# Kernel tuning notes

Measured on AMD Instinct MI355X. Metric: run time of the kernel, lower is better.

The kernel has to match this reference:

```python
import jax, jax.numpy as jnp
import numpy as np

B, D, H = 65536, 3, 256  # collocation batch, coord dim, hidden width


def setup_inputs() -> dict:
    key = jax.random.key(0)
    ks = jax.random.split(key, 8)

    def init(k, shape, fan_in):
        return jax.random.normal(k, shape, dtype=jnp.float32) * np.float32(1.0 / np.sqrt(fan_in))

    return {
        "x": jax.random.uniform(ks[0], (B, D), dtype=jnp.float32, minval=0.1, maxval=1.0),
        "W0": init(ks[1], (D, H), D), "b0": jnp.zeros((H,), jnp.float32),
        "W1": init(ks[2], (H, H), H), "b1": jnp.zeros((H,), jnp.float32),
        "W2": init(ks[3], (H, H), H), "b2": jnp.zeros((H,), jnp.float32),
        "W3": init(ks[4], (H, H), H), "b3": jnp.zeros((H,), jnp.float32),
        "Wout": init(ks[5], (H, 1), H), "bout": jnp.zeros((1,), jnp.float32),
    }


def reference(x, W0, b0, W1, b1, W2, b2, W3, b3, Wout, bout):
    # Scalar PINN network u(xi), xi: [D]
    def u_fn(xi):
        h = jnp.tanh(xi @ W0 + b0)
        h = jnp.tanh(h @ W1 + b1)
        h = jnp.tanh(h @ W2 + b2)
        h = jnp.tanh(h @ W3 + b3)
        return (h @ Wout + bout)[0]

    u = jax.vmap(u_fn)(x)                               # [B]
    # batch_gradient: du/dx_i for every coordinate axis (Cartesian: no adjustment)
    grads = jax.vmap(jax.grad(u_fn))(x)                 # [B, D]
    # batch_hessian diagonal: d^2u/dx_i^2 via forward-over-reverse
    hess_fn = jax.jacfwd(jax.grad(u_fn))                # [D, D] per sample
    hess_diag = jax.vmap(lambda xi: jnp.diagonal(hess_fn(xi)))(x)  # [B, D]
    # pack (u, grad, hessian-diagonal) as the PDE-residual ingredients
    return jnp.concatenate([u[:, None], grads, hess_diag], axis=1)  # [B, 1+D+D]
```

## Files before the change

kernel.cpp:

```cpp
#include <hip/hip_runtime.h>
#include <hip/hip_fp16.h>

#define HDIM 256
#define MS 16
#define LDAK 264
#define CSTRIDE (MS * LDAK * 2)

typedef _Float16 half8 __attribute__((ext_vector_type(8)));
typedef _Float16 half4 __attribute__((ext_vector_type(4)));
typedef _Float16 half2v __attribute__((ext_vector_type(2)));
typedef float f32x4 __attribute__((ext_vector_type(4)));

__device__ __forceinline__ float fast_tanh(float x) {
    float e = __expf(2.0f * x);
    return 1.0f - 2.0f * __builtin_amdgcn_rcpf(e + 1.0f);
}

__device__ __forceinline__ half4 cvt4(float a, float b, float c, float d) {
    half2v lo = __builtin_bit_cast(half2v, __builtin_amdgcn_cvt_pkrtz(a, b));
    half2v hi = __builtin_bit_cast(half2v, __builtin_amdgcn_cvt_pkrtz(c, d));
    half4 r; r[0] = lo[0]; r[1] = lo[1]; r[2] = hi[0]; r[3] = hi[1];
    return r;
}

__device__ __forceinline__ void barrier_lds() {
    asm volatile("s_waitcnt lgkmcnt(0)\n\ts_barrier" ::: "memory");
}

__global__ __launch_bounds__(256) void pack_weights(const float* __restrict__ W1,
                                                    const float* __restrict__ W2,
                                                    const float* __restrict__ W3,
                                                    _Float16* __restrict__ out) {
    int tid = blockIdx.x * 256 + threadIdx.x;
    int l = tid >> 13;
    int idx = tid & 8191;
    int kg = idx >> 8;
    int n = idx & 255;
    const float* W = (l == 0) ? W1 : (l == 1) ? W2 : W3;
    half8 v;
    #pragma unroll
    for (int j = 0; j < 8; ++j) v[j] = (_Float16)W[(kg * 8 + j) * 256 + n];
    *(half8*)(out + l * 65536 + kg * 2048 + n * 8) = v;
}

__global__ __launch_bounds__(256, 2)
void pinn_fused(const float* __restrict__ x,
                const float* __restrict__ W0,
                const float* __restrict__ b0,
                const float* __restrict__ b1,
                const float* __restrict__ b2,
                const float* __restrict__ b3,
                const float* __restrict__ Wout,
                const float* __restrict__ bout,
                const _Float16* __restrict__ Wp,
                float* __restrict__ out) {
    __shared__ __align__(16) _Float16 Abuf[7 * MS][LDAK];
    __shared__ float part[4 * 7 * MS];

    const int tid  = threadIdx.x;
    const int lane = tid & 63;
    const int wid  = tid >> 6;
    const int qd   = lane >> 4;
    const int n15  = lane & 15;
    const int base = blockIdx.x * MS;
    const int nw   = wid * 64 + n15;
    const int rot  = wid * 2;

    const _Float16* Wbase = Wp + (qd * 256 + nw) * 8;

    const char* Ab = (const char*)Abuf;
    const int abase = (n15 * LDAK + qd * 8) * 2;
    char* Sb = (char*)Abuf;
    const int sbase = (n15 * LDAK + wid * 64 + qd * 4) * 2;

    half8 wf[2][4];

#define PREFJ(JJ) do { \
    if ((JJ) < 24) { \
        const int g_ = (((JJ) >> 3) * 8 + ((rot + ((JJ) & 7)) & 7)); \
        _Pragma("unroll") \
        for (int t_ = 0; t_ < 4; ++t_) \
            wf[(JJ) & 1][t_] = *(const half8*)(Wbase + g_ * 8192 + t_ * 128); \
    } \
} while (0)

#define LDAFS(AF, I) do { \
    const int so_ = ((rot + (I)) & 7) * 64; \
    _Pragma("unroll") \
    for (int c_ = 0; c_ < 7; ++c_) \
        AF[c_] = *(const half8*)(Ab + abase + c_ * CSTRIDE + so_); \
} while (0)

#define MMSJ(ACC, AF, JJ) do { \
    PREFJ((JJ) + 1); \
    __builtin_amdgcn_s_setprio(1); \
    _Pragma("unroll") \
    for (int c_ = 0; c_ < 7; ++c_) \
        _Pragma("unroll") \
        for (int t_ = 0; t_ < 4; ++t_) \
            ACC[c_][t_] = __builtin_amdgcn_mfma_f32_16x16x32_f16(wf[(JJ) & 1][t_], AF[c_], ACC[c_][t_], 0, 0, 0); \
    __builtin_amdgcn_s_setprio(0); \
} while (0)

#define KPRE(ACC, L) do { \
    half8 afX[7], afY[7]; \
    LDAFS(afX, 0); LDAFS(afY, 1); \
    MMSJ(ACC, afX, (L) * 8 + 0); \
    MMSJ(ACC, afY, (L) * 8 + 1); \
} while (0)

#define KPOST(ACC, L) do { \
    half8 afX[7], afY[7]; \
    LDAFS(afX, 2); LDAFS(afY, 3); \
    MMSJ(ACC, afX, (L) * 8 + 2); LDAFS(afX, 4); \
    MMSJ(ACC, afY, (L) * 8 + 3); LDAFS(afY, 5); \
    MMSJ(ACC, afX, (L) * 8 + 4); LDAFS(afX, 6); \
    MMSJ(ACC, afY, (L) * 8 + 5); LDAFS(afY, 7); \
    MMSJ(ACC, afX, (L) * 8 + 6); \
    MMSJ(ACC, afY, (L) * 8 + 7); \
} while (0)

#define ZACC(A_) do { \
    _Pragma("unroll") \
    for (int c_ = 0; c_ < 7; ++c_) \
        _Pragma("unroll") \
        for (int t_ = 0; t_ < 4; ++t_) A_[c_][t_] = (f32x4){0.f, 0.f, 0.f, 0.f}; \
} while (0)

#define ELEMC(ACC, BB, EV) do { \
    _Pragma("unroll") \
    for (int tt_ = 0; tt_ < 4; ++tt_) { \
        const int ncol_ = wid * 64 + tt_ * 16 + qd * 4; \
        f32x4 bv_ = *(const f32x4*)((BB) + ncol_); \
        float tv_[4], gj_[3][4], sj_[3][4]; \
        _Pragma("unroll") \
        for (int r_ = 0; r_ < 4; ++r_) { \
            float zv_ = ACC[0][tt_][r_] + bv_[r_]; \
            tv_[r_] = fast_tanh(zv_); \
            float dd_ = 1.f - tv_[r_] * tv_[r_]; \
            float c2_ = -2.f * tv_[r_] * dd_; \
            _Pragma("unroll") \
            for (int i_ = 0; i_ < 3; ++i_) { \
                float zg_ = ACC[1 + i_][tt_][r_]; \
                float zs_ = ACC[4 + i_][tt_][r_]; \
                gj_[i_][r_] = dd_ * zg_; \
                sj_[i_][r_] = dd_ * zs_ + c2_ * zg_ * zg_; \
            } \
        } \
        EV[0][tt_] = cvt4(tv_[0], tv_[1], tv_[2], tv_[3]); \
        _Pragma("unroll") \
        for (int i_ = 0; i_ < 3; ++i_) { \
            EV[1 + i_][tt_] = cvt4(gj_[i_][0], gj_[i_][1], gj_[i_][2], gj_[i_][3]); \
            EV[4 + i_][tt_] = cvt4(sj_[i_][0], sj_[i_][1], sj_[i_][2], sj_[i_][3]); \
        } \
    } \
} while (0)

#define ELEMS(EV) do { \
    _Pragma("unroll") \
    for (int c_ = 0; c_ < 7; ++c_) \
        _Pragma("unroll") \
        for (int tt_ = 0; tt_ < 4; ++tt_) \
            *(half4*)(Sb + sbase + c_ * CSTRIDE + tt_ * 32) = EV[c_][tt_]; \
} while (0)

    f32x4 acc[7][4];
    half4 ev[7][4];

    ZACC(acc);
    PREFJ(0);

    {
        const int m  = tid & 15;
        const int nb = (tid >> 4) * 16;
        const float x0 = x[(base + m) * 3 + 0];
        const float x1 = x[(base + m) * 3 + 1];
        const float x2 = x[(base + m) * 3 + 2];
        #pragma unroll
        for (int ch = 0; ch < 2; ++ch) {
            const int n0 = nb + ch * 8;
            f32x4 w0v[2], w1v[2], w2v[2], bv[2];
            w0v[0] = *(const f32x4*)(W0 + n0);            w0v[1] = *(const f32x4*)(W0 + n0 + 4);
            w1v[0] = *(const f32x4*)(W0 + HDIM + n0);     w1v[1] = *(const f32x4*)(W0 + HDIM + n0 + 4);
            w2v[0] = *(const f32x4*)(W0 + 2 * HDIM + n0); w2v[1] = *(const f32x4*)(W0 + 2 * HDIM + n0 + 4);
            bv[0]  = *(const f32x4*)(b0 + n0);            bv[1]  = *(const f32x4*)(b0 + n0 + 4);
            half8 h[7];
            #pragma unroll
            for (int r = 0; r < 8; ++r) {
                const float w0 = w0v[r >> 2][r & 3];
                const float w1 = w1v[r >> 2][r & 3];
                const float w2 = w2v[r >> 2][r & 3];
                float z  = x0 * w0 + x1 * w1 + x2 * w2 + bv[r >> 2][r & 3];
                float tv = fast_tanh(z);
                float dd = 1.f - tv * tv;
                float c2 = -2.f * tv * dd;
                h[0][r] = (_Float16)tv;
                h[1][r] = (_Float16)(dd * w0);
                h[2][r] = (_Float16)(dd * w1);
                h[3][r] = (_Float16)(dd * w2);
                h[4][r] = (_Float16)(c2 * w0 * w0);
                h[5][r] = (_Float16)(c2 * w1 * w1);
                h[6][r] = (_Float16)(c2 * w2 * w2);
            }
            #pragma unroll
            for (int c = 0; c < 7; ++c)
                *(half8*)&Abuf[c * MS + m][n0] = h[c];
        }
    }
    KPRE(acc, 0);
    barrier_lds();

    KPOST(acc, 0);
    ELEMC(acc, b1, ev);
    barrier_lds();
    ELEMS(ev);
    ZACC(acc);
    KPRE(acc, 1);
    barrier_lds();

    KPOST(acc, 1);
    ELEMC(acc, b2, ev);
    barrier_lds();
    ELEMS(ev);
    ZACC(acc);
    KPRE(acc, 2);
    barrier_lds();

    KPOST(acc, 2);
    {
        float p[7] = {0.f, 0.f, 0.f, 0.f, 0.f, 0.f, 0.f};
        #pragma unroll
        for (int t = 0; t < 4; ++t) {
            const int ncol = wid * 64 + t * 16 + qd * 4;
            f32x4 bv = *(const f32x4*)(b3 + ncol);
            f32x4 wv = *(const f32x4*)(Wout + ncol);
            #pragma unroll
            for (int r = 0; r < 4; ++r) {
                float zv = acc[0][t][r] + bv[r];
                float tv = fast_tanh(zv);
                float dd = 1.f - tv * tv;
                float c2 = -2.f * tv * dd;
                p[0] += tv * wv[r];
                #pragma unroll
                for (int i = 0; i < 3; ++i) {
                    float zg = acc[1 + i][t][r];
                    float zs = acc[4 + i][t][r];
                    p[1 + i] += (dd * zg) * wv[r];
                    p[4 + i] += (dd * zs + c2 * zg * zg) * wv[r];
                }
            }
        }
        #pragma unroll
        for (int c = 0; c < 7; ++c) {
            p[c] += __shfl_xor(p[c], 16, 64);
            p[c] += __shfl_xor(p[c], 32, 64);
        }
        if (lane < 16) {
            #pragma unroll
            for (int c = 0; c < 7; ++c)
                part[(wid * 7 + c) * MS + lane] = p[c];
        }
    }
    barrier_lds();

    if (tid < 7 * MS) {
        const int c = tid >> 4;
        const int m = tid & 15;
        float v = part[(0 * 7 + c) * MS + m] + part[(1 * 7 + c) * MS + m] +
                  part[(2 * 7 + c) * MS + m] + part[(3 * 7 + c) * MS + m];
        if (c == 0) v += bout[0];
        out[(base + m) * 7 + c] = v;
    }

#undef PREFJ
#undef LDAFS
#undef MMSJ
#undef KPRE
#undef KPOST
#undef ZACC
#undef ELEMC
#undef ELEMS
}

extern "C" void kernel_launch(void* const* d_in, const int* in_sizes, int n_in,
                              void* d_out, int out_size, void* d_ws, size_t ws_size,
                              hipStream_t stream) {
    const float* xp   = (const float*)d_in[0];
    const float* W0   = (const float*)d_in[1];
    const float* b0   = (const float*)d_in[2];
    const float* W1   = (const float*)d_in[3];
    const float* b1   = (const float*)d_in[4];
    const float* W2   = (const float*)d_in[5];
    const float* b2   = (const float*)d_in[6];
    const float* W3   = (const float*)d_in[7];
    const float* b3   = (const float*)d_in[8];
    const float* Wout = (const float*)d_in[9];
    const float* bout = (const float*)d_in[10];
    _Float16* Wp = (_Float16*)d_ws;

    pack_weights<<<96, 256, 0, stream>>>(W1, W2, W3, Wp);
    pinn_fused<<<65536 / MS, 256, 0, stream>>>(xp, W0, b0, b1, b2, b3, Wout, bout, Wp,
                                               (float*)d_out);
}
```

Before: 246.6 us.

## Split hidden columns across eight waves per block instead of four

Doubles the block to 512 threads so each of eight waves computes 32 output columns per layer instead of 64. This halves per-wave accumulators and weight fragments, and the launch bounds now request 4 blocks per CU, aiming for more resident waves to hide latency. In exchange each wave reads the full A fragment from LDS for half the MFMA work, the software pipelining now holds one A buffer instead of two, and the final reduction sums eight partials.

```diff
diff --git a/kernel.cpp b/kernel.cpp
--- a/kernel.cpp
+++ b/kernel.cpp
@@ -43,7 +43,7 @@
     *(half8*)(out + l * 65536 + kg * 2048 + n * 8) = v;
 }
 
-__global__ __launch_bounds__(256, 2)
+__global__ __launch_bounds__(512, 4)
 void pinn_fused(const float* __restrict__ x,
                 const float* __restrict__ W0,
                 const float* __restrict__ b0,
@@ -55,7 +55,7 @@
                 const _Float16* __restrict__ Wp,
                 float* __restrict__ out) {
     __shared__ __align__(16) _Float16 Abuf[7 * MS][LDAK];
-    __shared__ float part[4 * 7 * MS];
+    __shared__ float part[8 * 7 * MS];
 
     const int tid  = threadIdx.x;
     const int lane = tid & 63;
@@ -63,23 +63,23 @@
     const int qd   = lane >> 4;
     const int n15  = lane & 15;
     const int base = blockIdx.x * MS;
-    const int nw   = wid * 64 + n15;
-    const int rot  = wid * 2;
+    const int nw   = wid * 32 + n15;
+    const int rot  = wid;
 
     const _Float16* Wbase = Wp + (qd * 256 + nw) * 8;
 
     const char* Ab = (const char*)Abuf;
     const int abase = (n15 * LDAK + qd * 8) * 2;
     char* Sb = (char*)Abuf;
-    const int sbase = (n15 * LDAK + wid * 64 + qd * 4) * 2;
-
-    half8 wf[2][4];
+    const int sbase = (n15 * LDAK + wid * 32 + qd * 4) * 2;
+
+    half8 wf[2][2];
 
 #define PREFJ(JJ) do { \
     if ((JJ) < 24) { \
         const int g_ = (((JJ) >> 3) * 8 + ((rot + ((JJ) & 7)) & 7)); \
         _Pragma("unroll") \
-        for (int t_ = 0; t_ < 4; ++t_) \
+        for (int t_ = 0; t_ < 2; ++t_) \
             wf[(JJ) & 1][t_] = *(const half8*)(Wbase + g_ * 8192 + t_ * 128); \
     } \
 } while (0)
@@ -97,40 +97,39 @@
     _Pragma("unroll") \
     for (int c_ = 0; c_ < 7; ++c_) \
         _Pragma("unroll") \
-        for (int t_ = 0; t_ < 4; ++t_) \
+        for (int t_ = 0; t_ < 2; ++t_) \
             ACC[c_][t_] = __builtin_amdgcn_mfma_f32_16x16x32_f16(wf[(JJ) & 1][t_], AF[c_], ACC[c_][t_], 0, 0, 0); \
     __builtin_amdgcn_s_setprio(0); \
 } while (0)
 
 #define KPRE(ACC, L) do { \
-    half8 afX[7], afY[7]; \
-    LDAFS(afX, 0); LDAFS(afY, 1); \
-    MMSJ(ACC, afX, (L) * 8 + 0); \
-    MMSJ(ACC, afY, (L) * 8 + 1); \
+    half8 af_[7]; \
+    LDAFS(af_, 0); \
+    MMSJ(ACC, af_, (L) * 8 + 0); \
 } while (0)
 
 #define KPOST(ACC, L) do { \
-    half8 afX[7], afY[7]; \
-    LDAFS(afX, 2); LDAFS(afY, 3); \
-    MMSJ(ACC, afX, (L) * 8 + 2); LDAFS(afX, 4); \
-    MMSJ(ACC, afY, (L) * 8 + 3); LDAFS(afY, 5); \
-    MMSJ(ACC, afX, (L) * 8 + 4); LDAFS(afX, 6); \
-    MMSJ(ACC, afY, (L) * 8 + 5); LDAFS(afY, 7); \
-    MMSJ(ACC, afX, (L) * 8 + 6); \
-    MMSJ(ACC, afY, (L) * 8 + 7); \
+    half8 af_[7]; \
+    LDAFS(af_, 1); MMSJ(ACC, af_, (L) * 8 + 1); \
+    LDAFS(af_, 2); MMSJ(ACC, af_, (L) * 8 + 2); \
+    LDAFS(af_, 3); MMSJ(ACC, af_, (L) * 8 + 3); \
+    LDAFS(af_, 4); MMSJ(ACC, af_, (L) * 8 + 4); \
+    LDAFS(af_, 5); MMSJ(ACC, af_, (L) * 8 + 5); \
+    LDAFS(af_, 6); MMSJ(ACC, af_, (L) * 8 + 6); \
+    LDAFS(af_, 7); MMSJ(ACC, af_, (L) * 8 + 7); \
 } while (0)
 
 #define ZACC(A_) do { \
     _Pragma("unroll") \
     for (int c_ = 0; c_ < 7; ++c_) \
         _Pragma("unroll") \
-        for (int t_ = 0; t_ < 4; ++t_) A_[c_][t_] = (f32x4){0.f, 0.f, 0.f, 0.f}; \
+        for (int t_ = 0; t_ < 2; ++t_) A_[c_][t_] = (f32x4){0.f, 0.f, 0.f, 0.f}; \
 } while (0)
 
 #define ELEMC(ACC, BB, EV) do { \
     _Pragma("unroll") \
-    for (int tt_ = 0; tt_ < 4; ++tt_) { \
-        const int ncol_ = wid * 64 + tt_ * 16 + qd * 4; \
+    for (int tt_ = 0; tt_ < 2; ++tt_) { \
+        const int ncol_ = wid * 32 + tt_ * 16 + qd * 4; \
         f32x4 bv_ = *(const f32x4*)((BB) + ncol_); \
         float tv_[4], gj_[3][4], sj_[3][4]; \
         _Pragma("unroll") \
@@ -160,52 +159,48 @@
     _Pragma("unroll") \
     for (int c_ = 0; c_ < 7; ++c_) \
         _Pragma("unroll") \
-        for (int tt_ = 0; tt_ < 4; ++tt_) \
+        for (int tt_ = 0; tt_ < 2; ++tt_) \
             *(half4*)(Sb + sbase + c_ * CSTRIDE + tt_ * 32) = EV[c_][tt_]; \
 } while (0)
 
-    f32x4 acc[7][4];
-    half4 ev[7][4];
+    f32x4 acc[7][2];
+    half4 ev[7][2];
 
     ZACC(acc);
     PREFJ(0);
 
     {
         const int m  = tid & 15;
-        const int nb = (tid >> 4) * 16;
+        const int n0 = (tid >> 4) * 8;
         const float x0 = x[(base + m) * 3 + 0];
         const float x1 = x[(base + m) * 3 + 1];
         const float x2 = x[(base + m) * 3 + 2];
-        #pragma unroll
-        for (int ch = 0; ch < 2; ++ch) {
-            const int n0 = nb + ch * 8;
-            f32x4 w0v[2], w1v[2], w2v[2], bv[2];
-            w0v[0] = *(const f32x4*)(W0 + n0);            w0v[1] = *(const f32x4*)(W0 + n0 + 4);
-            w1v[0] = *(const f32x4*)(W0 + HDIM + n0);     w1v[1] = *(const f32x4*)(W0 + HDIM + n0 + 4);
-            w2v[0] = *(const f32x4*)(W0 + 2 * HDIM + n0); w2v[1] = *(const f32x4*)(W0 + 2 * HDIM + n0 + 4);
-            bv[0]  = *(const f32x4*)(b0 + n0);            bv[1]  = *(const f32x4*)(b0 + n0 + 4);
-            half8 h[7];
-            #pragma unroll
-            for (int r = 0; r < 8; ++r) {
-                const float w0 = w0v[r >> 2][r & 3];
-                const float w1 = w1v[r >> 2][r & 3];
-                const float w2 = w2v[r >> 2][r & 3];
-                float z  = x0 * w0 + x1 * w1 + x2 * w2 + bv[r >> 2][r & 3];
-                float tv = fast_tanh(z);
-                float dd = 1.f - tv * tv;
-                float c2 = -2.f * tv * dd;
-                h[0][r] = (_Float16)tv;
-                h[1][r] = (_Float16)(dd * w0);
-                h[2][r] = (_Float16)(dd * w1);
-                h[3][r] = (_Float16)(dd * w2);
-                h[4][r] = (_Float16)(c2 * w0 * w0);
-                h[5][r] = (_Float16)(c2 * w1 * w1);
-                h[6][r] = (_Float16)(c2 * w2 * w2);
-            }
-            #pragma unroll
-            for (int c = 0; c < 7; ++c)
-                *(half8*)&Abuf[c * MS + m][n0] = h[c];
+        f32x4 w0v[2], w1v[2], w2v[2], bv[2];
+        w0v[0] = *(const f32x4*)(W0 + n0);            w0v[1] = *(const f32x4*)(W0 + n0 + 4);
+        w1v[0] = *(const f32x4*)(W0 + HDIM + n0);     w1v[1] = *(const f32x4*)(W0 + HDIM + n0 + 4);
+        w2v[0] = *(const f32x4*)(W0 + 2 * HDIM + n0); w2v[1] = *(const f32x4*)(W0 + 2 * HDIM + n0 + 4);
+        bv[0]  = *(const f32x4*)(b0 + n0);            bv[1]  = *(const f32x4*)(b0 + n0 + 4);
+        half8 h[7];
+        #pragma unroll
+        for (int r = 0; r < 8; ++r) {
+            const float w0 = w0v[r >> 2][r & 3];
+            const float w1 = w1v[r >> 2][r & 3];
+            const float w2 = w2v[r >> 2][r & 3];
+            float z  = x0 * w0 + x1 * w1 + x2 * w2 + bv[r >> 2][r & 3];
+            float tv = fast_tanh(z);
+            float dd = 1.f - tv * tv;
+            float c2 = -2.f * tv * dd;
+            h[0][r] = (_Float16)tv;
+            h[1][r] = (_Float16)(dd * w0);
+            h[2][r] = (_Float16)(dd * w1);
+            h[3][r] = (_Float16)(dd * w2);
+            h[4][r] = (_Float16)(c2 * w0 * w0);
+            h[5][r] = (_Float16)(c2 * w1 * w1);
+            h[6][r] = (_Float16)(c2 * w2 * w2);
         }
+        #pragma unroll
+        for (int c = 0; c < 7; ++c)
+            *(half8*)&Abuf[c * MS + m][n0] = h[c];
     }
     KPRE(acc, 0);
     barrier_lds();
@@ -230,8 +225,8 @@
     {
         float p[7] = {0.f, 0.f, 0.f, 0.f, 0.f, 0.f, 0.f};
         #pragma unroll
-        for (int t = 0; t < 4; ++t) {
-            const int ncol = wid * 64 + t * 16 + qd * 4;
+        for (int t = 0; t < 2; ++t) {
+            const int ncol = wid * 32 + t * 16 + qd * 4;
             f32x4 bv = *(const f32x4*)(b3 + ncol);
             f32x4 wv = *(const f32x4*)(Wout + ncol);
             #pragma unroll
@@ -266,8 +261,9 @@
     if (tid < 7 * MS) {
         const int c = tid >> 4;
         const int m = tid & 15;
-        float v = part[(0 * 7 + c) * MS + m] + part[(1 * 7 + c) * MS + m] +
-                  part[(2 * 7 + c) * MS + m] + part[(3 * 7 + c) * MS + m];
+        float v = 0.f;
+        #pragma unroll
+        for (int w = 0; w < 8; ++w) v += part[(w * 7 + c) * MS + m];
         if (c == 0) v += bout[0];
         out[(base + m) * 7 + c] = v;
     }
@@ -299,6 +295,6 @@
     _Float16* Wp = (_Float16*)d_ws;
 
     pack_weights<<<96, 256, 0, stream>>>(W1, W2, W3, Wp);
-    pinn_fused<<<65536 / MS, 256, 0, stream>>>(xp, W0, b0, b1, b2, b3, Wout, bout, Wp,
+    pinn_fused<<<65536 / MS, 512, 0, stream>>>(xp, W0, b0, b1, b2, b3, Wout, bout, Wp,
                                                (float*)d_out);
 }
```

Result: slower. 281.6 us (+14.2%).
